# Optimization experiments

Hardware: AMD Instinct MI355X
Metric: run time of the kernel (lower is better)

The kernel has to match this reference:

```python
import jax, jax.numpy as jnp
import numpy as np

B, ND, NE, D, H = 2, 2048, 2048, 1024, 16
HD = D // H
DFF = 4 * D
EPS = 1e-5


def setup_inputs() -> dict:
    key = jax.random.key(0)
    ks = jax.random.split(key, 16)
    s = lambda fan_in: 1.0 / np.sqrt(fan_in)
    inp = {
        'x': jax.random.normal(ks[0], (B, ND, D), jnp.float32),
        'memory': jax.random.normal(ks[1], (B, NE, D), jnp.float32),
        'ln1_g': jnp.ones((D,), jnp.float32), 'ln1_b': jnp.zeros((D,), jnp.float32),
        'Wqkv': jax.random.normal(ks[2], (D, 3 * D), jnp.float32) * s(D),
        'Wo_sa': jax.random.normal(ks[3], (D, D), jnp.float32) * s(D),
        'bo_sa': jnp.zeros((D,), jnp.float32),
        'ln2_g': jnp.ones((D,), jnp.float32), 'ln2_b': jnp.zeros((D,), jnp.float32),
        'Wq': jax.random.normal(ks[4], (D, D), jnp.float32) * s(D),
        'Wk': jax.random.normal(ks[5], (D, D), jnp.float32) * s(D),
        'Wv': jax.random.normal(ks[6], (D, D), jnp.float32) * s(D),
        'Wo_ca': jax.random.normal(ks[7], (D, D), jnp.float32) * s(D),
        'bo_ca': jnp.zeros((D,), jnp.float32),
        'ln3_g': jnp.ones((D,), jnp.float32), 'ln3_b': jnp.zeros((D,), jnp.float32),
        'W1': jax.random.normal(ks[8], (D, DFF), jnp.float32) * s(D),
        'b1': jnp.zeros((DFF,), jnp.float32),
        'W2': jax.random.normal(ks[9], (DFF, D), jnp.float32) * s(DFF),
        'b2': jnp.zeros((D,), jnp.float32),
        'attn_mask': jnp.tril(jnp.ones((ND, ND), jnp.bool_)),
    }
    return inp


def _layernorm(x, g, b):
    mu = jnp.mean(x, axis=-1, keepdims=True)
    var = jnp.mean(jnp.square(x - mu), axis=-1, keepdims=True)
    return (x - mu) * jax.lax.rsqrt(var + EPS) * g + b


def _heads(t, n):  # (B,N,D) -> (B,H,N,HD)
    Bn = t.shape[0]
    return t.reshape(Bn, n, H, HD).transpose(0, 2, 1, 3)


def _attend(q, k, v, mask=None):
    scale = HD ** -0.5
    scores = jnp.einsum('bhqd,bhkd->bhqk', q, k) * scale
    if mask is not None:
        scores = jnp.where(mask, scores, -jnp.inf)
    attn = jax.nn.softmax(scores, axis=-1)
    out = jnp.einsum('bhqk,bhkd->bhqd', attn, v)
    Bn, _, Nq, _ = out.shape
    return out.transpose(0, 2, 1, 3).reshape(Bn, Nq, D)


def reference(x, memory, ln1_g, ln1_b, Wqkv, Wo_sa, bo_sa, ln2_g, ln2_b,
              Wq, Wk, Wv, Wo_ca, bo_ca, ln3_g, ln3_b, W1, b1, W2, b2, attn_mask):
    # --- masked self-attention ---
    h = _layernorm(x, ln1_g, ln1_b)
    qkv = (h @ Wqkv).reshape(B, ND, 3, H, HD).transpose(2, 0, 3, 1, 4)  # (3,B,H,N,HD)
    q, k, v = qkv[0], qkv[1], qkv[2]
    sa = _attend(q, k, v, attn_mask[None, None]) @ Wo_sa + bo_sa
    x = x + sa
    # --- cross-attention ---
    h = _layernorm(x, ln2_g, ln2_b)
    q = _heads(h @ Wq, ND)
    k = _heads(memory @ Wk, NE)
    v = _heads(memory @ Wv, NE)
    ca = _attend(q, k, v) @ Wo_ca + bo_ca
    x = x + ca
    # --- FFN ---
    h = _layernorm(x, ln3_g, ln3_b)
    x = x + (jax.nn.gelu(h @ W1 + b1, approximate=False) @ W2 + b2)
    return x
```

## Files before the change

### kernel.cpp

```cpp
#include <hip/hip_runtime.h>
#include <hip/hip_bf16.h>
#include <math.h>

#define B_   2
#define ND_  2048
#define NE_  2048
#define D_   1024
#define H_   16
#define HD_  64
#define DFF_ 4096
#define T_   4096

typedef __attribute__((ext_vector_type(8))) short bf16x8;
typedef __attribute__((ext_vector_type(4))) float f32x4;

#if __has_builtin(__builtin_amdgcn_exp2f)
#define EXP2(x) __builtin_amdgcn_exp2f(x)
#else
#define EXP2(x) exp2f(x)
#endif

__device__ __forceinline__ short f2bf(float f) {
  union { float f; unsigned u; } v; v.f = f;
  return (short)((v.u + 0x7FFFu + ((v.u >> 16) & 1u)) >> 16);
}
__device__ __forceinline__ float bf2f(short s) {
  union { unsigned u; float f; } v; v.u = ((unsigned)(unsigned short)s) << 16;
  return v.f;
}

typedef const __attribute__((address_space(1))) void gvoid_t;
typedef __attribute__((address_space(3))) void lvoid_t;

__device__ __forceinline__ void gload16(const void* src, void* dst) {
  __builtin_amdgcn_global_load_lds((gvoid_t*)src, (lvoid_t*)dst, 16, 0, 0);
}

__global__ __launch_bounds__(256) void wt_cast(const float* __restrict__ in,
                                               short* __restrict__ out,
                                               int K, int N) {
  __shared__ float t[32][33];
  const int tx = threadIdx.x, ty = threadIdx.y;
  const int n0 = blockIdx.x * 32, k0 = blockIdx.y * 32;
#pragma unroll
  for (int i = 0; i < 4; ++i)
    t[ty + i * 8][tx] = in[(size_t)(k0 + ty + i * 8) * N + n0 + tx];
  __syncthreads();
#pragma unroll
  for (int i = 0; i < 4; ++i)
    out[(size_t)(n0 + ty + i * 8) * K + k0 + tx] = f2bf(t[tx][ty + i * 8]);
}

__global__ __launch_bounds__(256) void wt_cast5(const float* __restrict__ i0,
                                                const float* __restrict__ i1,
                                                const float* __restrict__ i2,
                                                const float* __restrict__ i3,
                                                const float* __restrict__ i4,
                                                short* __restrict__ o0,
                                                short* __restrict__ o1,
                                                short* __restrict__ o2,
                                                short* __restrict__ o3,
                                                short* __restrict__ o4) {
  const int z = blockIdx.z;
  const float* in = z == 0 ? i0 : z == 1 ? i1 : z == 2 ? i2 : z == 3 ? i3 : i4;
  short* out      = z == 0 ? o0 : z == 1 ? o1 : z == 2 ? o2 : z == 3 ? o3 : o4;
  __shared__ float t[32][33];
  const int tx = threadIdx.x, ty = threadIdx.y;
  const int n0 = blockIdx.x * 32, k0 = blockIdx.y * 32;
#pragma unroll
  for (int i = 0; i < 4; ++i)
    t[ty + i * 8][tx] = in[(size_t)(k0 + ty + i * 8) * 1024 + n0 + tx];
  __syncthreads();
#pragma unroll
  for (int i = 0; i < 4; ++i)
    out[(size_t)(n0 + ty + i * 8) * 1024 + k0 + tx] = f2bf(t[tx][ty + i * 8]);
}

__global__ __launch_bounds__(256) void castf2b(const float* __restrict__ in,
                                               short* __restrict__ out) {
  const int i = blockIdx.x * 256 + threadIdx.x;
  float4 v = ((const float4*)in)[i];
  short4 o;
  o.x = f2bf(v.x); o.y = f2bf(v.y); o.z = f2bf(v.z); o.w = f2bf(v.w);
  ((short4*)out)[i] = o;
}

__global__ __launch_bounds__(256) void ln_kernel(const float* __restrict__ x,
                                                 const float* __restrict__ g,
                                                 const float* __restrict__ b,
                                                 short* __restrict__ out) {
  const int row = blockIdx.x;
  const int tid = threadIdx.x;
  const float* xr = x + (size_t)row * D_;
  float4 v = reinterpret_cast<const float4*>(xr)[tid];
  float s  = v.x + v.y + v.z + v.w;
  float s2 = v.x * v.x + v.y * v.y + v.z * v.z + v.w * v.w;
#pragma unroll
  for (int m = 1; m < 64; m <<= 1) {
    s  += __shfl_xor(s, m);
    s2 += __shfl_xor(s2, m);
  }
  __shared__ float ss[4], ss2[4];
  const int w = tid >> 6;
  if ((tid & 63) == 0) { ss[w] = s; ss2[w] = s2; }
  __syncthreads();
  s  = ss[0] + ss[1] + ss[2] + ss[3];
  s2 = ss2[0] + ss2[1] + ss2[2] + ss2[3];
  const float mu   = s * (1.0f / D_);
  const float var  = s2 * (1.0f / D_) - mu * mu;
  const float rstd = rsqrtf(var + 1e-5f);
  float4 gv = reinterpret_cast<const float4*>(g)[tid];
  float4 bv = reinterpret_cast<const float4*>(b)[tid];
  short4 o;
  o.x = f2bf((v.x - mu) * rstd * gv.x + bv.x);
  o.y = f2bf((v.y - mu) * rstd * gv.y + bv.y);
  o.z = f2bf((v.z - mu) * rstd * gv.z + bv.z);
  o.w = f2bf((v.w - mu) * rstd * gv.w + bv.w);
  reinterpret_cast<short4*>(out + (size_t)row * D_)[tid] = o;
}

__global__ __launch_bounds__(256) void ln_fused(const float* __restrict__ xprev,
                                                const short* delta,
                                                const float* __restrict__ pbias,
                                                const float* __restrict__ g,
                                                const float* __restrict__ b,
                                                short* out_ln,
                                                float* __restrict__ out_x) {
  const int row = blockIdx.x;
  const int tid = threadIdx.x;
  float4 v = reinterpret_cast<const float4*>(xprev + (size_t)row * D_)[tid];
  short4 dv = reinterpret_cast<const short4*>(delta + (size_t)row * D_)[tid];
  float4 pb = reinterpret_cast<const float4*>(pbias)[tid];
  v.x += bf2f(dv.x) + pb.x;
  v.y += bf2f(dv.y) + pb.y;
  v.z += bf2f(dv.z) + pb.z;
  v.w += bf2f(dv.w) + pb.w;
  float s  = v.x + v.y + v.z + v.w;
  float s2 = v.x * v.x + v.y * v.y + v.z * v.z + v.w * v.w;
#pragma unroll
  for (int m = 1; m < 64; m <<= 1) {
    s  += __shfl_xor(s, m);
    s2 += __shfl_xor(s2, m);
  }
  __shared__ float ss[4], ss2[4];
  const int w = tid >> 6;
  if ((tid & 63) == 0) { ss[w] = s; ss2[w] = s2; }
  __syncthreads();
  s  = ss[0] + ss[1] + ss[2] + ss[3];
  s2 = ss2[0] + ss2[1] + ss2[2] + ss2[3];
  const float mu   = s * (1.0f / D_);
  const float var  = s2 * (1.0f / D_) - mu * mu;
  const float rstd = rsqrtf(var + 1e-5f);
  reinterpret_cast<float4*>(out_x + (size_t)row * D_)[tid] = v;
  float4 gv = reinterpret_cast<const float4*>(g)[tid];
  float4 bv = reinterpret_cast<const float4*>(b)[tid];
  short4 o;
  o.x = f2bf((v.x - mu) * rstd * gv.x + bv.x);
  o.y = f2bf((v.y - mu) * rstd * gv.y + bv.y);
  o.z = f2bf((v.z - mu) * rstd * gv.z + bv.z);
  o.w = f2bf((v.w - mu) * rstd * gv.w + bv.w);
  reinterpret_cast<short4*>(out_ln + (size_t)row * D_)[tid] = o;
}

__global__ __launch_bounds__(256) void addbias(const float* __restrict__ x,
                                               const short* __restrict__ delta,
                                               const float* __restrict__ bias,
                                               float* __restrict__ out) {
  const int i = blockIdx.x * 256 + threadIdx.x;
  float4 v = ((const float4*)x)[i];
  short4 dv = ((const short4*)delta)[i];
  const int col = (i * 4) & (D_ - 1);
  float4 pb = *(const float4*)(bias + col);
  v.x += bf2f(dv.x) + pb.x;
  v.y += bf2f(dv.y) + pb.y;
  v.z += bf2f(dv.z) + pb.z;
  v.w += bf2f(dv.w) + pb.w;
  ((float4*)out)[i] = v;
}

template <int MODE>
__global__ __launch_bounds__(256) void gemm_bt(const short* __restrict__ A,
                                               const short* __restrict__ Bt,
                                               const float* __restrict__ bias,
                                               void* __restrict__ Cout,
                                               int M, int N, int K) {
  __shared__ short As[128 * 32];
  __shared__ short Bs[128 * 32];
  const int tid = threadIdx.x;
  const int gx = gridDim.x;
  const int nwg = gx * gridDim.y;
  int lin = blockIdx.y * gx + blockIdx.x;
  lin = (lin & 7) * (nwg >> 3) + (lin >> 3);
  const int m0 = (lin / gx) * 128, n0 = (lin % gx) * 128;
  const int wave = tid >> 6, lane = tid & 63;
  const int wm = (wave >> 1) * 64, wn = (wave & 1) * 64;
  const int lr = lane & 15, lg = lane >> 4;

  f32x4 acc[4][4];
#pragma unroll
  for (int i = 0; i < 4; ++i)
#pragma unroll
    for (int j = 0; j < 4; ++j) acc[i][j] = f32x4{0.f, 0.f, 0.f, 0.f};

  const int e0 = tid * 8, e1 = 2048 + tid * 8;
  const int r0 = e0 >> 5, c0 = e0 & 31;
  const int r1 = e1 >> 5, c1 = e1 & 31;
  const size_t ar0 = (size_t)(m0 + r0) * K, ar1 = (size_t)(m0 + r1) * K;
  const size_t br0 = (size_t)(n0 + r0) * K, br1 = (size_t)(n0 + r1) * K;

  for (int k0 = 0; k0 < K; k0 += 32) {
    gload16(A + ar0 + k0 + c0, As + e0);
    gload16(A + ar1 + k0 + c1, As + e1);
    gload16(Bt + br0 + k0 + c0, Bs + e0);
    gload16(Bt + br1 + k0 + c1, Bs + e1);
    __syncthreads();
    bf16x8 af[4], bfr[4];
#pragma unroll
    for (int mi = 0; mi < 4; ++mi)
      af[mi] = *(const bf16x8*)(As + (wm + mi * 16 + lr) * 32 + lg * 8);
#pragma unroll
    for (int ni = 0; ni < 4; ++ni)
      bfr[ni] = *(const bf16x8*)(Bs + (wn + ni * 16 + lr) * 32 + lg * 8);
#pragma unroll
    for (int mi = 0; mi < 4; ++mi)
#pragma unroll
      for (int ni = 0; ni < 4; ++ni)
        acc[mi][ni] = __builtin_amdgcn_mfma_f32_16x16x32_bf16(
            af[mi], bfr[ni], acc[mi][ni], 0, 0, 0);
    __syncthreads();
  }

#pragma unroll
  for (int mi = 0; mi < 4; ++mi) {
    const int row = m0 + wm + mi * 16 + lg * 4;
#pragma unroll
    for (int ni = 0; ni < 4; ++ni) {
      const int col = n0 + wn + ni * 16 + lr;
#pragma unroll
      for (int r = 0; r < 4; ++r) {
        const size_t idx = (size_t)(row + r) * N + col;
        const float v = acc[mi][ni][r];
        if (MODE == 0) {
          ((short*)Cout)[idx] = f2bf(v);
        } else {
          const float tt = v + bias[col];
          const float yy = fmaf(tt * tt * tt, 0.044715f, tt);
          const float e = EXP2(yy * -2.3022343813918633f);
          ((short*)Cout)[idx] = f2bf(tt / (1.0f + e));
        }
      }
    }
  }
}

__global__ __launch_bounds__(256) void gemm_bt3(const short* __restrict__ A0,
                                                const short* __restrict__ A1,
                                                const short* __restrict__ A2,
                                                const short* __restrict__ B0,
                                                const short* __restrict__ B1,
                                                const short* __restrict__ B2,
                                                short* __restrict__ C0,
                                                short* __restrict__ C1,
                                                short* __restrict__ C2,
                                                int M, int N, int K) {
  const int z = blockIdx.z;
  const short* A  = z == 0 ? A0 : (z == 1 ? A1 : A2);
  const short* Bt = z == 0 ? B0 : (z == 1 ? B1 : B2);
  short* C        = z == 0 ? C0 : (z == 1 ? C1 : C2);

  __shared__ short As[128 * 32];
  __shared__ short Bs[128 * 32];
  const int tid = threadIdx.x;
  const int gx = gridDim.x;
  const int nwg = gx * gridDim.y;
  int lin = blockIdx.y * gx + blockIdx.x;
  lin = (lin & 7) * (nwg >> 3) + (lin >> 3);
  const int m0 = (lin / gx) * 128, n0 = (lin % gx) * 128;
  const int wave = tid >> 6, lane = tid & 63;
  const int wm = (wave >> 1) * 64, wn = (wave & 1) * 64;
  const int lr = lane & 15, lg = lane >> 4;

  f32x4 acc[4][4];
#pragma unroll
  for (int i = 0; i < 4; ++i)
#pragma unroll
    for (int j = 0; j < 4; ++j) acc[i][j] = f32x4{0.f, 0.f, 0.f, 0.f};

  const int e0 = tid * 8, e1 = 2048 + tid * 8;
  const int r0 = e0 >> 5, c0 = e0 & 31;
  const int r1 = e1 >> 5, c1 = e1 & 31;
  const size_t ar0 = (size_t)(m0 + r0) * K, ar1 = (size_t)(m0 + r1) * K;
  const size_t br0 = (size_t)(n0 + r0) * K, br1 = (size_t)(n0 + r1) * K;

  for (int k0 = 0; k0 < K; k0 += 32) {
    gload16(A + ar0 + k0 + c0, As + e0);
    gload16(A + ar1 + k0 + c1, As + e1);
    gload16(Bt + br0 + k0 + c0, Bs + e0);
    gload16(Bt + br1 + k0 + c1, Bs + e1);
    __syncthreads();
    bf16x8 af[4], bfr[4];
#pragma unroll
    for (int mi = 0; mi < 4; ++mi)
      af[mi] = *(const bf16x8*)(As + (wm + mi * 16 + lr) * 32 + lg * 8);
#pragma unroll
    for (int ni = 0; ni < 4; ++ni)
      bfr[ni] = *(const bf16x8*)(Bs + (wn + ni * 16 + lr) * 32 + lg * 8);
#pragma unroll
    for (int mi = 0; mi < 4; ++mi)
#pragma unroll
      for (int ni = 0; ni < 4; ++ni)
        acc[mi][ni] = __builtin_amdgcn_mfma_f32_16x16x32_bf16(
            af[mi], bfr[ni], acc[mi][ni], 0, 0, 0);
    __syncthreads();
  }

#pragma unroll
  for (int mi = 0; mi < 4; ++mi) {
    const int row = m0 + wm + mi * 16 + lg * 4;
#pragma unroll
    for (int ni = 0; ni < 4; ++ni) {
      const int col = n0 + wn + ni * 16 + lr;
#pragma unroll
      for (int r = 0; r < 4; ++r)
        C[(size_t)(row + r) * N + col] = f2bf(acc[mi][ni][r]);
    }
  }
}

__global__ __launch_bounds__(256) void gemm_bt64(const short* __restrict__ A,
                                                 const short* __restrict__ Bt,
                                                 short* __restrict__ Cout,
                                                 int M, int N, int K) {
  __shared__ short As[64 * 32];
  __shared__ short Bs[128 * 32];
  const int tid = threadIdx.x;
  const int gx = gridDim.x;
  const int nwg = gx * gridDim.y;
  int lin = blockIdx.y * gx + blockIdx.x;
  lin = (lin & 7) * (nwg >> 3) + (lin >> 3);
  const int m0 = (lin / gx) * 64, n0 = (lin % gx) * 128;
  const int wave = tid >> 6, lane = tid & 63;
  const int wn = wave * 32;
  const int lr = lane & 15, lg = lane >> 4;

  f32x4 acc[4][2];
#pragma unroll
  for (int i = 0; i < 4; ++i)
#pragma unroll
    for (int j = 0; j < 2; ++j) acc[i][j] = f32x4{0.f, 0.f, 0.f, 0.f};

  const int ea = tid * 8;
  const int ra = ea >> 5, ca = ea & 31;
  const int e0 = tid * 8, e1 = 2048 + tid * 8;
  const int r0 = e0 >> 5, c0 = e0 & 31;
  const int r1 = e1 >> 5, c1 = e1 & 31;
  const size_t ar = (size_t)(m0 + ra) * K;
  const size_t br0 = (size_t)(n0 + r0) * K, br1 = (size_t)(n0 + r1) * K;

  for (int k0 = 0; k0 < K; k0 += 32) {
    gload16(A + ar + k0 + ca, As + ea);
    gload16(Bt + br0 + k0 + c0, Bs + e0);
    gload16(Bt + br1 + k0 + c1, Bs + e1);
    __syncthreads();
    bf16x8 af[4], bfr[2];
#pragma unroll
    for (int mi = 0; mi < 4; ++mi)
      af[mi] = *(const bf16x8*)(As + (mi * 16 + lr) * 32 + lg * 8);
#pragma unroll
    for (int ni = 0; ni < 2; ++ni)
      bfr[ni] = *(const bf16x8*)(Bs + (wn + ni * 16 + lr) * 32 + lg * 8);
#pragma unroll
    for (int mi = 0; mi < 4; ++mi)
#pragma unroll
      for (int ni = 0; ni < 2; ++ni)
        acc[mi][ni] = __builtin_amdgcn_mfma_f32_16x16x32_bf16(
            af[mi], bfr[ni], acc[mi][ni], 0, 0, 0);
    __syncthreads();
  }

#pragma unroll
  for (int mi = 0; mi < 4; ++mi) {
    const int row = m0 + mi * 16 + lg * 4;
#pragma unroll
    for (int ni = 0; ni < 2; ++ni) {
      const int col = n0 + wn + ni * 16 + lr;
#pragma unroll
      for (int r = 0; r < 4; ++r)
        Cout[(size_t)(row + r) * N + col] = f2bf(acc[mi][ni][r]);
    }
  }
}

__global__ __launch_bounds__(256) void vtrans(const short* __restrict__ in,
                                              short* __restrict__ out,
                                              int ldi, int N) {
  const int bh = blockIdx.z;
  const int b = bh >> 4, h = bh & 15;
  const short* ib = in + (size_t)b * N * ldi + h * HD_;
  short* ob = out + (size_t)bh * HD_ * N;
  __shared__ short t[32][33];
  const int tx = threadIdx.x, ty = threadIdx.y;
  const int n0 = blockIdx.x * 32, d0 = blockIdx.y * 32;
#pragma unroll
  for (int i = 0; i < 4; ++i)
    t[ty + i * 8][tx] = ib[(size_t)(n0 + ty + i * 8) * ldi + d0 + tx];
  __syncthreads();
#pragma unroll
  for (int i = 0; i < 4; ++i)
    ob[(size_t)(d0 + ty + i * 8) * N + n0 + tx] = t[tx][ty + i * 8];
}

__global__ __launch_bounds__(256) void flash(const short* __restrict__ Q,
                                             const short* __restrict__ Kp,
                                             const short* __restrict__ Vt,
                                             short* __restrict__ O,
                                             int ldq, int ldk, int ldo,
                                             int NK, int causal) {
  const int bh = blockIdx.x;
  int qb = blockIdx.y;
  if (causal) qb = (qb < 16) ? (2 * qb) : (63 - 2 * qb);
  const int b = bh >> 4, h = bh & 15;
  const int q0 = qb * 64;
  const int tid = threadIdx.x, wave = tid >> 6, lane = tid & 63;
  const int lr = lane & 15, lg = lane >> 4;
  const int lx = lr & 7;

  const short* Qb = Q + (size_t)b * ND_ * ldq + h * HD_;
  const short* Kb = Kp + (size_t)b * NK * ldk + h * HD_;
  const short* Vb = Vt + (size_t)bh * HD_ * NK;
  short* Ob = O + (size_t)b * ND_ * ldo + h * HD_;

  __shared__ short Ks[64 * 64];
  __shared__ short Vs[64 * 64];
  __shared__ short Ps[4][16 * 64];

  const int qrow = q0 + wave * 16 + lr;
  const bf16x8 qf0 = *(const bf16x8*)(Qb + (size_t)qrow * ldq + lg * 8);
  const bf16x8 qf1 = *(const bf16x8*)(Qb + (size_t)qrow * ldq + 32 + lg * 8);

  const bf16x8 ONES = {0x3F80, 0x3F80, 0x3F80, 0x3F80,
                       0x3F80, 0x3F80, 0x3F80, 0x3F80};

  f32x4 oacc[4];
  f32x4 lacc = f32x4{0.f, 0.f, 0.f, 0.f};
  float m_own = -1e30f;
#pragma unroll
  for (int i = 0; i < 4; ++i) oacc[i] = f32x4{0.f, 0.f, 0.f, 0.f};

  const int sr0 = tid >> 3;
  const int ssw = ((tid & 7) ^ (sr0 & 7)) * 8;
  const int e0 = tid * 8, e1 = 2048 + tid * 8;

  const float SC = 0.18033688011112042f;

  short* Pw = &Ps[wave][0];
  const int pbase = lr * 64 + (lg & 1) * 4;

  const int nkt = causal ? (qb + 1) : (NK / 64);
  for (int t = 0; t < nkt; ++t) {
    const int k0 = t * 64;
    gload16(Kb + (size_t)(k0 + sr0) * ldk + ssw, Ks + e0);
    gload16(Kb + (size_t)(k0 + 32 + sr0) * ldk + ssw, Ks + e1);
    gload16(Vb + (size_t)sr0 * NK + k0 + ssw, Vs + e0);
    gload16(Vb + (size_t)(32 + sr0) * NK + k0 + ssw, Vs + e1);
    __syncthreads();

    f32x4 st[4];
#pragma unroll
    for (int kb = 0; kb < 4; ++kb) {
      const bf16x8 kf0 = *(const bf16x8*)(Ks + (kb * 16 + lr) * 64 + ((lg ^ lx) * 8));
      const bf16x8 kf1 = *(const bf16x8*)(Ks + (kb * 16 + lr) * 64 + (((4 + lg) ^ lx) * 8));
      st[kb] = f32x4{0.f, 0.f, 0.f, 0.f};
      st[kb] = __builtin_amdgcn_mfma_f32_16x16x32_bf16(kf0, qf0, st[kb], 0, 0, 0);
      st[kb] = __builtin_amdgcn_mfma_f32_16x16x32_bf16(kf1, qf1, st[kb], 0, 0, 0);
    }
    if (causal && t == nkt - 1) {
#pragma unroll
      for (int kb = 0; kb < 4; ++kb)
#pragma unroll
        for (int r = 0; r < 4; ++r)
          if ((k0 + kb * 16 + lg * 4 + r) > qrow) st[kb][r] = -3.0e38f;
    }

    float rm = st[0][0];
#pragma unroll
    for (int kb = 0; kb < 4; ++kb)
#pragma unroll
      for (int r = 0; r < 4; ++r)
        if (kb || r) rm = fmaxf(rm, st[kb][r]);
    rm = fmaxf(rm, __shfl_xor(rm, 16));
    rm = fmaxf(rm, __shfl_xor(rm, 32));

    if (!__all(rm - m_own <= 44.f)) {
      const float nm = fmaxf(m_own, rm);
      const float fac = EXP2((m_own - nm) * SC);
      m_own = nm;
      const float fr0 = __shfl(fac, (lg << 2) + 0);
      const float fr1 = __shfl(fac, (lg << 2) + 1);
      const float fr2 = __shfl(fac, (lg << 2) + 2);
      const float fr3 = __shfl(fac, (lg << 2) + 3);
#pragma unroll
      for (int db = 0; db < 4; ++db) {
        oacc[db][0] *= fr0; oacc[db][1] *= fr1;
        oacc[db][2] *= fr2; oacc[db][3] *= fr3;
      }
      lacc[0] *= fr0; lacc[1] *= fr1; lacc[2] *= fr2; lacc[3] *= fr3;
    }
    const float nmsc = m_own * SC;
#pragma unroll
    for (int kb = 0; kb < 4; ++kb)
#pragma unroll
      for (int r = 0; r < 4; ++r)
        st[kb][r] = EXP2(fmaf(st[kb][r], SC, -nmsc));

#pragma unroll
    for (int kb = 0; kb < 4; ++kb) {
      union { unsigned u[2]; unsigned long long ull; } pk;
      asm("v_cvt_pk_bf16_f32 %0, %1, %2"
          : "=v"(pk.u[0]) : "v"(st[kb][0]), "v"(st[kb][1]));
      asm("v_cvt_pk_bf16_f32 %0, %1, %2"
          : "=v"(pk.u[1]) : "v"(st[kb][2]), "v"(st[kb][3]));
      const int cs = kb * 2 + (lg >> 1);
      *(unsigned long long*)(Pw + pbase + ((cs ^ lx) * 8)) = pk.ull;
    }
    const bf16x8 pf0 = *(const bf16x8*)(Pw + lr * 64 + ((lg ^ lx) * 8));
    const bf16x8 pf1 = *(const bf16x8*)(Pw + lr * 64 + (((4 + lg) ^ lx) * 8));

#pragma unroll
    for (int db = 0; db < 4; ++db) {
      const bf16x8 vf0 = *(const bf16x8*)(Vs + (db * 16 + lr) * 64 + ((lg ^ lx) * 8));
      const bf16x8 vf1 = *(const bf16x8*)(Vs + (db * 16 + lr) * 64 + (((4 + lg) ^ lx) * 8));
      oacc[db] = __builtin_amdgcn_mfma_f32_16x16x32_bf16(pf0, vf0, oacc[db], 0, 0, 0);
      oacc[db] = __builtin_amdgcn_mfma_f32_16x16x32_bf16(pf1, vf1, oacc[db], 0, 0, 0);
    }
    lacc = __builtin_amdgcn_mfma_f32_16x16x32_bf16(pf0, ONES, lacc, 0, 0, 0);
    lacc = __builtin_amdgcn_mfma_f32_16x16x32_bf16(pf1, ONES, lacc, 0, 0, 0);
    __syncthreads();
  }
#pragma unroll
  for (int db = 0; db < 4; ++db)
#pragma unroll
    for (int r = 0; r < 4; ++r) {
      const int q = q0 + wave * 16 + lg * 4 + r;
      Ob[(size_t)q * ldo + db * 16 + lr] = f2bf(oacc[db][r] / lacc[r]);
    }
}

extern "C" void kernel_launch(void* const* d_in, const int* in_sizes, int n_in,
                              void* d_out, int out_size, void* d_ws, size_t ws_size,
                              hipStream_t stream) {
  const float* x      = (const float*)d_in[0];
  const float* memory = (const float*)d_in[1];
  const float* ln1_g  = (const float*)d_in[2];
  const float* ln1_b  = (const float*)d_in[3];
  const float* Wqkv   = (const float*)d_in[4];
  const float* Wo_sa  = (const float*)d_in[5];
  const float* bo_sa  = (const float*)d_in[6];
  const float* ln2_g  = (const float*)d_in[7];
  const float* ln2_b  = (const float*)d_in[8];
  const float* Wq     = (const float*)d_in[9];
  const float* Wk     = (const float*)d_in[10];
  const float* Wv     = (const float*)d_in[11];
  const float* Wo_ca  = (const float*)d_in[12];
  const float* bo_ca  = (const float*)d_in[13];
  const float* ln3_g  = (const float*)d_in[14];
  const float* ln3_b  = (const float*)d_in[15];
  const float* W1     = (const float*)d_in[16];
  const float* b1     = (const float*)d_in[17];
  const float* W2     = (const float*)d_in[18];
  const float* b2     = (const float*)d_in[19];

  char* ws = (char*)d_ws;
  size_t o = 0;
  auto alloc = [&](size_t bytes) { char* p = ws + o; o += bytes; return p; };
  short* wqkv_t = (short*)alloc((size_t)3072 * 1024 * 2);
  short* wosa_t = (short*)alloc((size_t)1024 * 1024 * 2);
  short* wq_t   = (short*)alloc((size_t)1024 * 1024 * 2);
  short* wk_t   = (short*)alloc((size_t)1024 * 1024 * 2);
  short* wv_t   = (short*)alloc((size_t)1024 * 1024 * 2);
  short* woca_t = (short*)alloc((size_t)1024 * 1024 * 2);
  short* w1_t   = (short*)alloc((size_t)4096 * 1024 * 2);
  short* w2_t   = (short*)alloc((size_t)1024 * 4096 * 2);
  short* hbf    = (short*)alloc((size_t)T_ * 1024 * 2);
  short* bufa   = (short*)alloc((size_t)T_ * 3072 * 2);
  short* vt     = (short*)alloc((size_t)32 * 64 * 2048 * 2);
  short* attn   = (short*)alloc((size_t)T_ * 1024 * 2);
  short* membf  = (short*)alloc((size_t)T_ * 1024 * 2);
  float* x1     = (float*)alloc((size_t)T_ * 1024 * 4);
  float* x2     = (float*)alloc((size_t)T_ * 1024 * 4);
  if (o > ws_size) return;

  short* ffn = bufa;
  short* qca = bufa;
  short* kca = bufa + (size_t)T_ * 1024;
  short* vca = bufa + (size_t)2 * T_ * 1024;

  const dim3 tb(32, 8);

  wt_cast<<<dim3(3072 / 32, 1024 / 32), tb, 0, stream>>>(Wqkv, wqkv_t, 1024, 3072);
  wt_cast5<<<dim3(32, 32, 5), tb, 0, stream>>>(Wo_sa, Wq, Wk, Wv, Wo_ca,
                                               wosa_t, wq_t, wk_t, wv_t, woca_t);
  wt_cast<<<dim3(4096 / 32, 1024 / 32), tb, 0, stream>>>(W1, w1_t, 1024, 4096);
  wt_cast<<<dim3(1024 / 32, 4096 / 32), tb, 0, stream>>>(W2, w2_t, 4096, 1024);
  castf2b<<<dim3((T_ * 1024) / (256 * 4)), 256, 0, stream>>>(memory, membf);

  ln_kernel<<<dim3(T_), 256, 0, stream>>>(x, ln1_g, ln1_b, hbf);
  gemm_bt<0><<<dim3(3072 / 128, T_ / 128), 256, 0, stream>>>(
      hbf, wqkv_t, nullptr, bufa, T_, 3072, 1024);
  vtrans<<<dim3(ND_ / 32, HD_ / 32, 32), tb, 0, stream>>>(bufa + 2048, vt, 3072, ND_);
  flash<<<dim3(32, ND_ / 64), 256, 0, stream>>>(
      bufa, bufa + 1024, vt, attn, 3072, 3072, 1024, ND_, 1);
  gemm_bt64<<<dim3(1024 / 128, T_ / 64), 256, 0, stream>>>(
      attn, wosa_t, hbf, T_, 1024, 1024);
  ln_fused<<<dim3(T_), 256, 0, stream>>>(x, hbf, bo_sa, ln2_g, ln2_b, hbf, x1);

  gemm_bt3<<<dim3(1024 / 128, T_ / 128, 3), 256, 0, stream>>>(
      hbf, membf, membf, wq_t, wk_t, wv_t, qca, kca, vca, T_, 1024, 1024);
  vtrans<<<dim3(NE_ / 32, HD_ / 32, 32), tb, 0, stream>>>(vca, vt, 1024, NE_);
  flash<<<dim3(32, ND_ / 64), 256, 0, stream>>>(
      qca, kca, vt, attn, 1024, 1024, 1024, NE_, 0);
  gemm_bt64<<<dim3(1024 / 128, T_ / 64), 256, 0, stream>>>(
      attn, woca_t, hbf, T_, 1024, 1024);
  ln_fused<<<dim3(T_), 256, 0, stream>>>(x1, hbf, bo_ca, ln3_g, ln3_b, hbf, x2);

  gemm_bt<2><<<dim3(4096 / 128, T_ / 128), 256, 0, stream>>>(
      hbf, w1_t, b1, ffn, T_, 4096, 1024);
  gemm_bt64<<<dim3(1024 / 128, T_ / 64), 256, 0, stream>>>(
      ffn, w2_t, hbf, T_, 1024, 4096);
  addbias<<<dim3((T_ * 1024) / (256 * 4)), 256, 0, stream>>>(
      x2, hbf, b2, (float*)d_out);
}
```

Before: 421.1 us.

## Double-buffer LDS tiles in the bt64 GEMM and attention kernels

Both the gemm_bt64 kernel and the flash-attention kernel now keep two shared-memory buffers for their staged tiles. Each loop iteration issues global-to-LDS loads for the next K/V or A/B tile before computing on the current one, which leaves one barrier per iteration instead of two. The aim is to hide global load latency behind the MFMA work. In exchange the shared-memory footprint grows, which can lower how many workgroups fit on each compute unit.

After: 411.6 us. -2.3%, faster.

```diff
diff --git a/kernel.cpp b/kernel.cpp
--- a/kernel.cpp
+++ b/kernel.cpp
@@ -331,8 +331,8 @@
                                                  const short* __restrict__ Bt,
                                                  short* __restrict__ Cout,
                                                  int M, int N, int K) {
-  __shared__ short As[64 * 32];
-  __shared__ short Bs[128 * 32];
+  __shared__ short As[2][64 * 32];
+  __shared__ short Bs[2][128 * 32];
   const int tid = threadIdx.x;
   const int gx = gridDim.x;
   const int nwg = gx * gridDim.y;
@@ -357,18 +357,26 @@
   const size_t ar = (size_t)(m0 + ra) * K;
   const size_t br0 = (size_t)(n0 + r0) * K, br1 = (size_t)(n0 + r1) * K;
 
+  auto stage = [&](int buf, int k0) {
+    gload16(A + ar + k0 + ca, &As[buf][0] + ea);
+    gload16(Bt + br0 + k0 + c0, &Bs[buf][0] + e0);
+    gload16(Bt + br1 + k0 + c1, &Bs[buf][0] + e1);
+  };
+
+  stage(0, 0);
+  __syncthreads();
+  int cur = 0;
   for (int k0 = 0; k0 < K; k0 += 32) {
-    gload16(A + ar + k0 + ca, As + ea);
-    gload16(Bt + br0 + k0 + c0, Bs + e0);
-    gload16(Bt + br1 + k0 + c1, Bs + e1);
-    __syncthreads();
+    if (k0 + 32 < K) stage(cur ^ 1, k0 + 32);
+    const short* Ab = &As[cur][0];
+    const short* Bb = &Bs[cur][0];
     bf16x8 af[4], bfr[2];
 #pragma unroll
     for (int mi = 0; mi < 4; ++mi)
-      af[mi] = *(const bf16x8*)(As + (mi * 16 + lr) * 32 + lg * 8);
+      af[mi] = *(const bf16x8*)(Ab + (mi * 16 + lr) * 32 + lg * 8);
 #pragma unroll
     for (int ni = 0; ni < 2; ++ni)
-      bfr[ni] = *(const bf16x8*)(Bs + (wn + ni * 16 + lr) * 32 + lg * 8);
+      bfr[ni] = *(const bf16x8*)(Bb + (wn + ni * 16 + lr) * 32 + lg * 8);
 #pragma unroll
     for (int mi = 0; mi < 4; ++mi)
 #pragma unroll
@@ -376,6 +384,7 @@
         acc[mi][ni] = __builtin_amdgcn_mfma_f32_16x16x32_bf16(
             af[mi], bfr[ni], acc[mi][ni], 0, 0, 0);
     __syncthreads();
+    cur ^= 1;
   }
 
 #pragma unroll
@@ -430,8 +439,8 @@
   const short* Vb = Vt + (size_t)bh * HD_ * NK;
   short* Ob = O + (size_t)b * ND_ * ldo + h * HD_;
 
-  __shared__ short Ks[64 * 64];
-  __shared__ short Vs[64 * 64];
+  __shared__ short Ks[2][64 * 64];
+  __shared__ short Vs[2][64 * 64];
   __shared__ short Ps[4][16 * 64];
 
   const int qrow = q0 + wave * 16 + lr;
@@ -456,20 +465,28 @@
   short* Pw = &Ps[wave][0];
   const int pbase = lr * 64 + (lg & 1) * 4;
 
+  auto stage = [&](int buf, int k0) {
+    gload16(Kb + (size_t)(k0 + sr0) * ldk + ssw, &Ks[buf][0] + e0);
+    gload16(Kb + (size_t)(k0 + 32 + sr0) * ldk + ssw, &Ks[buf][0] + e1);
+    gload16(Vb + (size_t)sr0 * NK + k0 + ssw, &Vs[buf][0] + e0);
+    gload16(Vb + (size_t)(32 + sr0) * NK + k0 + ssw, &Vs[buf][0] + e1);
+  };
+
   const int nkt = causal ? (qb + 1) : (NK / 64);
+  stage(0, 0);
+  __syncthreads();
+  int cur = 0;
   for (int t = 0; t < nkt; ++t) {
     const int k0 = t * 64;
-    gload16(Kb + (size_t)(k0 + sr0) * ldk + ssw, Ks + e0);
-    gload16(Kb + (size_t)(k0 + 32 + sr0) * ldk + ssw, Ks + e1);
-    gload16(Vb + (size_t)sr0 * NK + k0 + ssw, Vs + e0);
-    gload16(Vb + (size_t)(32 + sr0) * NK + k0 + ssw, Vs + e1);
-    __syncthreads();
+    if (t + 1 < nkt) stage(cur ^ 1, k0 + 64);
+    const short* Ksb = &Ks[cur][0];
+    const short* Vsb = &Vs[cur][0];
 
     f32x4 st[4];
 #pragma unroll
     for (int kb = 0; kb < 4; ++kb) {
-      const bf16x8 kf0 = *(const bf16x8*)(Ks + (kb * 16 + lr) * 64 + ((lg ^ lx) * 8));
-      const bf16x8 kf1 = *(const bf16x8*)(Ks + (kb * 16 + lr) * 64 + (((4 + lg) ^ lx) * 8));
+      const bf16x8 kf0 = *(const bf16x8*)(Ksb + (kb * 16 + lr) * 64 + ((lg ^ lx) * 8));
+      const bf16x8 kf1 = *(const bf16x8*)(Ksb + (kb * 16 + lr) * 64 + (((4 + lg) ^ lx) * 8));
       st[kb] = f32x4{0.f, 0.f, 0.f, 0.f};
       st[kb] = __builtin_amdgcn_mfma_f32_16x16x32_bf16(kf0, qf0, st[kb], 0, 0, 0);
       st[kb] = __builtin_amdgcn_mfma_f32_16x16x32_bf16(kf1, qf1, st[kb], 0, 0, 0);
@@ -528,14 +545,15 @@
 
 #pragma unroll
     for (int db = 0; db < 4; ++db) {
-      const bf16x8 vf0 = *(const bf16x8*)(Vs + (db * 16 + lr) * 64 + ((lg ^ lx) * 8));
-      const bf16x8 vf1 = *(const bf16x8*)(Vs + (db * 16 + lr) * 64 + (((4 + lg) ^ lx) * 8));
+      const bf16x8 vf0 = *(const bf16x8*)(Vsb + (db * 16 + lr) * 64 + ((lg ^ lx) * 8));
+      const bf16x8 vf1 = *(const bf16x8*)(Vsb + (db * 16 + lr) * 64 + (((4 + lg) ^ lx) * 8));
       oacc[db] = __builtin_amdgcn_mfma_f32_16x16x32_bf16(pf0, vf0, oacc[db], 0, 0, 0);
       oacc[db] = __builtin_amdgcn_mfma_f32_16x16x32_bf16(pf1, vf1, oacc[db], 0, 0, 0);
     }
     lacc = __builtin_amdgcn_mfma_f32_16x16x32_bf16(pf0, ONES, lacc, 0, 0, 0);
     lacc = __builtin_amdgcn_mfma_f32_16x16x32_bf16(pf1, ONES, lacc, 0, 0, 0);
     __syncthreads();
+    cur ^= 1;
   }
 #pragma unroll
   for (int db = 0; db < 4; ++db)
```
